# Performance work log

Measured on AMD Instinct MI355X. Metric: run time of the kernel, lower is better.

## Reference

```python
import jax, jax.numpy as jnp
import numpy as np

ALPHA = 0.2  # LeakyReLU negative slope
B, L, FIN, FOUT = 128, 512, 128, 128

def setup_inputs() -> dict:
    key = jax.random.key(0)
    k1, k2, k3, k4, k5 = jax.random.split(key, 5)
    h = jax.random.normal(k1, (B, L, FIN), jnp.float32)
    W = jax.random.normal(k2, (FIN, FOUT), jnp.float32) * (1.0 / np.sqrt(FIN))
    a = jax.random.normal(k3, (2 * FOUT,), jnp.float32) * (1.0 / np.sqrt(2 * FOUT))
    edge_bias = jax.random.normal(k4, (B, L, L), jnp.float32) * 0.1
    adj_mask = jax.random.uniform(k5, (L, L)) > 0.3
    adj_mask = adj_mask | jnp.eye(L, dtype=bool)  # self-loops avoid fully-masked rows
    return {"h": h, "W": W, "a": a, "edge_bias": edge_bias, "adj_mask": adj_mask}

def reference(h, W, a, edge_bias, adj_mask):
    # Wh: [B, L, Fout]
    Wh = jnp.einsum('blf,fo->blo', h, W)
    Fout = W.shape[1]
    # a([Wh_i, Wh_j]) == Wh_i @ a[:Fout] + Wh_j @ a[Fout:]  (avoids O(B*L*L*2F) concat)
    ei = Wh @ a[:Fout]   # [B, L]  (target i contribution)
    ej = Wh @ a[Fout:]   # [B, L]  (source j contribution)
    e = jax.nn.leaky_relu(ei[:, :, None] + ej[:, None, :], ALPHA) + edge_bias  # [B, L, L]
    e = jnp.where(adj_mask[None, :, :], e, -jnp.inf)
    att = jax.nn.softmax(e, axis=-1)  # dropout=0.0 -> identity
    h_prime = jnp.einsum('bij,bjo->bio', att, Wh)  # [B, L, Fout]
    return jax.nn.elu(h_prime)  # concat=True branch
```

## Files before the change

kernel.cpp:

```cpp
#include <hip/hip_runtime.h>
#include <string.h>

#define ALPHA 0.2f

typedef short short8 __attribute__((ext_vector_type(8)));
typedef float floatx4 __attribute__((ext_vector_type(4)));
typedef int intx4 __attribute__((ext_vector_type(4)));
typedef unsigned short ushort4v __attribute__((ext_vector_type(4)));

__device__ inline unsigned short f2bf(float f) {
    unsigned int v; __builtin_memcpy(&v, &f, 4);
    v = v + 0x7FFFu + ((v >> 16) & 1u);
    return (unsigned short)(v >> 16);
}

__global__ __launch_bounds__(256) void wh_kernel(const float* __restrict__ h,
                                                 const float* __restrict__ W,
                                                 const float* __restrict__ a,
                                                 unsigned short* __restrict__ wht,
                                                 float* __restrict__ ei,
                                                 float* __restrict__ ej)
{
    __shared__ __align__(16) unsigned short h_s[128][136];
    __shared__ __align__(16) unsigned short w_s[128][136];
    __shared__ float a_s[256];
    const int tid  = threadIdx.x;
    const int lane = tid & 63;
    const int wv   = tid >> 6;
    const int quad = lane >> 4;
    const int l16  = lane & 15;
    const int r0   = blockIdx.x * 128;
    const int b    = r0 >> 9;
    const int jb   = r0 & 511;

    const float* hbase = h + (size_t)r0 * 128;
    for (int it = 0; it < 16; ++it) {
        int idx4 = it * 256 + tid;
        floatx4 v = *(const floatx4*)(hbase + idx4 * 4);
        int row = idx4 >> 5;
        int col = (idx4 & 31) * 4;
        ushort4v u;
        for (int e = 0; e < 4; ++e) u[e] = f2bf(v[e]);
        *(ushort4v*)&h_s[row][col] = u;
    }
    for (int it = 0; it < 64; ++it) {
        int idx = it * 256 + tid;
        w_s[idx & 127][idx >> 7] = f2bf(W[idx]);
    }
    a_s[tid] = a[tid];
    __syncthreads();

    floatx4 acc[8][2];
    for (int mo = 0; mo < 8; ++mo)
        for (int n = 0; n < 2; ++n) acc[mo][n] = (floatx4)0.f;

    for (int kk = 0; kk < 4; ++kk) {
        short8 bfr[2];
        for (int n = 0; n < 2; ++n)
            bfr[n] = *(const short8*)&h_s[wv * 32 + n * 16 + l16][kk * 32 + quad * 8];
        for (int mo = 0; mo < 8; ++mo) {
            short8 afr = *(const short8*)&w_s[mo * 16 + l16][kk * 32 + quad * 8];
            acc[mo][0] = __builtin_amdgcn_mfma_f32_16x16x32_bf16(afr, bfr[0], acc[mo][0], 0, 0, 0);
            acc[mo][1] = __builtin_amdgcn_mfma_f32_16x16x32_bf16(afr, bfr[1], acc[mo][1], 0, 0, 0);
        }
    }

    for (int n = 0; n < 2; ++n) {
        float si = 0.f, sj = 0.f;
        for (int mo = 0; mo < 8; ++mo)
            for (int r = 0; r < 4; ++r) {
                int o = mo * 16 + quad * 4 + r;
                float v = acc[mo][n][r];
                si += v * a_s[o];
                sj += v * a_s[128 + o];
            }
        si += __shfl_xor(si, 16); si += __shfl_xor(si, 32);
        sj += __shfl_xor(sj, 16); sj += __shfl_xor(sj, 32);
        if (quad == 0) {
            int j = jb + wv * 32 + n * 16 + l16;
            ei[b * 512 + j] = si;
            ej[b * 512 + j] = sj;
        }
    }

    for (int mo = 0; mo < 8; ++mo)
        for (int n = 0; n < 2; ++n)
            for (int r = 0; r < 4; ++r) {
                int o = mo * 16 + quad * 4 + r;
                int j = jb + wv * 32 + n * 16 + l16;
                wht[(size_t)b * 65536 + o * 512 + j] = f2bf(acc[mo][n][r]);
            }
}

__global__ __launch_bounds__(256, 4) void attn_kernel(const unsigned short* __restrict__ wht,
                                                      const float* __restrict__ ei,
                                                      const float* __restrict__ ej,
                                                      const float* __restrict__ bias,
                                                      const int* __restrict__ adj,
                                                      float* __restrict__ out)
{
    __shared__ __align__(16) unsigned short p_s[32][520];
    __shared__ float ei_s[32];
    __shared__ float s_row[32];

    const int tid  = threadIdx.x;
    const int lane = tid & 63;
    const int wv   = tid >> 6;
    const int quad = lane >> 4;
    const int l16  = lane & 15;
    const int b    = blockIdx.x >> 4;
    const int i0   = (blockIdx.x & 15) * 32;

    const floatx4 ejv0 = *(const floatx4*)(ej + b * 512 + lane * 4);
    const floatx4 ejv1 = *(const floatx4*)(ej + b * 512 + 256 + lane * 4);
    if (tid < 32) ei_s[tid] = ei[b * 512 + i0 + tid];
    __syncthreads();

    const float* bp = bias + ((size_t)(b * 512 + i0 + wv * 8)) * 512;
    const int*   ap = adj + (i0 + wv * 8) * 512;
    floatx4 bb0 = *(const floatx4*)(bp + lane * 4);
    floatx4 bb1 = *(const floatx4*)(bp + 256 + lane * 4);
    intx4   mm0 = *(const intx4*)(ap + lane * 4);
    intx4   mm1 = *(const intx4*)(ap + 256 + lane * 4);

    float rsum[8];

#pragma unroll
    for (int rr = 0; rr < 8; ++rr) {
        floatx4 nb0, nb1; intx4 nm0, nm1;
        if (rr < 7) {
            nb0 = *(const floatx4*)(bp + 512 + lane * 4);
            nb1 = *(const floatx4*)(bp + 768 + lane * 4);
            nm0 = *(const intx4*)(ap + 512 + lane * 4);
            nm1 = *(const intx4*)(ap + 768 + lane * 4);
        }
        const int il = wv * 8 + rr;
        const float eiv = ei_s[il];
        float sm = 0.f;
        ushort4v p0, p1;
        for (int e = 0; e < 4; ++e) {
            float x = eiv + ejv0[e];
            x = fmaxf(x, ALPHA * x);
            x += bb0[e];
            float p = __expf(x);
            p = (mm0[e] != 0) ? p : 0.f;
            sm += p;
            p0[e] = f2bf(p);
        }
        for (int e = 0; e < 4; ++e) {
            float x = eiv + ejv1[e];
            x = fmaxf(x, ALPHA * x);
            x += bb1[e];
            float p = __expf(x);
            p = (mm1[e] != 0) ? p : 0.f;
            sm += p;
            p1[e] = f2bf(p);
        }
        *(ushort4v*)&p_s[il][lane * 4]       = p0;
        *(ushort4v*)&p_s[il][256 + lane * 4] = p1;
        rsum[rr] = sm;
        bb0 = nb0; bb1 = nb1; mm0 = nm0; mm1 = nm1;
        bp += 512; ap += 512;
    }

#pragma unroll
    for (int rr = 0; rr < 8; ++rr)
        for (int off = 32; off; off >>= 1)
            rsum[rr] += __shfl_xor(rsum[rr], off);
    if (lane == 0)
#pragma unroll
        for (int rr = 0; rr < 8; ++rr) s_row[wv * 8 + rr] = rsum[rr];
    __syncthreads();

    floatx4 acc[2][2];
    for (int m = 0; m < 2; ++m)
        for (int n = 0; n < 2; ++n) acc[m][n] = (floatx4)0.f;

    const unsigned short* wbase = wht + (size_t)b * 65536;
    const unsigned short* wb0 = wbase + (wv * 32 + l16) * 512 + quad * 8;
    const unsigned short* wb1 = wbase + (wv * 32 + 16 + l16) * 512 + quad * 8;
    short8 bf0 = *(const short8*)(wb0);
    short8 bf1 = *(const short8*)(wb1);
#pragma unroll
    for (int k16 = 0; k16 < 16; ++k16) {
        int ko = k16 * 32 + quad * 8;
        short8 nbf0, nbf1;
        if (k16 < 15) {
            nbf0 = *(const short8*)(wb0 + (k16 + 1) * 32);
            nbf1 = *(const short8*)(wb1 + (k16 + 1) * 32);
        }
        short8 af0 = *(const short8*)&p_s[l16][ko];
        short8 af1 = *(const short8*)&p_s[16 + l16][ko];
        acc[0][0] = __builtin_amdgcn_mfma_f32_16x16x32_bf16(af0, bf0, acc[0][0], 0, 0, 0);
        acc[0][1] = __builtin_amdgcn_mfma_f32_16x16x32_bf16(af0, bf1, acc[0][1], 0, 0, 0);
        acc[1][0] = __builtin_amdgcn_mfma_f32_16x16x32_bf16(af1, bf0, acc[1][0], 0, 0, 0);
        acc[1][1] = __builtin_amdgcn_mfma_f32_16x16x32_bf16(af1, bf1, acc[1][1], 0, 0, 0);
        bf0 = nbf0; bf1 = nbf1;
    }

    for (int m = 0; m < 2; ++m)
        for (int n = 0; n < 2; ++n)
            for (int r = 0; r < 4; ++r) {
                int il = m * 16 + quad * 4 + r;
                int o  = wv * 32 + n * 16 + l16;
                float v = acc[m][n][r] / s_row[il];
                v = v > 0.f ? v : (__expf(v) - 1.f);
                out[((size_t)(b * 512 + i0 + il)) * 128 + o] = v;
            }
}

extern "C" void kernel_launch(void* const* d_in, const int* in_sizes, int n_in,
                              void* d_out, int out_size, void* d_ws, size_t ws_size,
                              hipStream_t stream)
{
    const float* h    = (const float*)d_in[0];
    const float* W    = (const float*)d_in[1];
    const float* a    = (const float*)d_in[2];
    const float* bias = (const float*)d_in[3];
    const int*   adj  = (const int*)d_in[4];
    float*       out  = (float*)d_out;

    unsigned short* wht = (unsigned short*)d_ws;
    float* ei = (float*)((char*)d_ws + 16777216);
    float* ej = ei + 65536;

    hipLaunchKernelGGL(wh_kernel,   dim3(512),  dim3(256), 0, stream, h, W, a, wht, ei, ej);
    hipLaunchKernelGGL(attn_kernel, dim3(2048), dim3(256), 0, stream, wht, ei, ej, bias, adj, out);
}
```

Before: 262.3 us.

## Double threads per block and add nontemporal loads/stores for streamed data

Both kernels move from 256 to 512 threads per block, so each wave handles half as many rows/columns (4 attention rows instead of 8, one 16-column MFMA tile instead of two), with launch bounds raised for occupancy. Streaming inputs (h, edge_bias) use nontemporal loads and the output uses nontemporal stores to reduce cache pollution. The bias/adj prefetch is also issued before the first barrier so it overlaps the ei/ej loads. More waves add latency hiding at the cost of less per-wave reuse of the P fragments and W^T loads.

```diff
diff --git a/kernel.cpp b/kernel.cpp
--- a/kernel.cpp
+++ b/kernel.cpp
@@ -14,12 +14,16 @@
     return (unsigned short)(v >> 16);
 }
 
-__global__ __launch_bounds__(256) void wh_kernel(const float* __restrict__ h,
-                                                 const float* __restrict__ W,
-                                                 const float* __restrict__ a,
-                                                 unsigned short* __restrict__ wht,
-                                                 float* __restrict__ ei,
-                                                 float* __restrict__ ej)
+__device__ inline floatx4 ntload_f4(const float* p) {
+    return __builtin_nontemporal_load((const floatx4*)p);
+}
+
+__global__ __launch_bounds__(512, 4) void wh_kernel(const float* __restrict__ h,
+                                                    const float* __restrict__ W,
+                                                    const float* __restrict__ a,
+                                                    unsigned short* __restrict__ wht,
+                                                    float* __restrict__ ei,
+                                                    float* __restrict__ ej)
 {
     __shared__ __align__(16) unsigned short h_s[128][136];
     __shared__ __align__(16) unsigned short w_s[128][136];
@@ -34,65 +38,67 @@
     const int jb   = r0 & 511;
 
     const float* hbase = h + (size_t)r0 * 128;
-    for (int it = 0; it < 16; ++it) {
-        int idx4 = it * 256 + tid;
-        floatx4 v = *(const floatx4*)(hbase + idx4 * 4);
+#pragma unroll
+    for (int it = 0; it < 8; ++it) {
+        int idx4 = it * 512 + tid;
+        floatx4 v = ntload_f4(hbase + idx4 * 4);
         int row = idx4 >> 5;
         int col = (idx4 & 31) * 4;
         ushort4v u;
         for (int e = 0; e < 4; ++e) u[e] = f2bf(v[e]);
         *(ushort4v*)&h_s[row][col] = u;
     }
-    for (int it = 0; it < 64; ++it) {
-        int idx = it * 256 + tid;
+#pragma unroll
+    for (int it = 0; it < 32; ++it) {
+        int idx = it * 512 + tid;
         w_s[idx & 127][idx >> 7] = f2bf(W[idx]);
     }
-    a_s[tid] = a[tid];
+    if (tid < 256) a_s[tid] = a[tid];
     __syncthreads();
 
-    floatx4 acc[8][2];
-    for (int mo = 0; mo < 8; ++mo)
-        for (int n = 0; n < 2; ++n) acc[mo][n] = (floatx4)0.f;
-
+    floatx4 acc[8];
+#pragma unroll
+    for (int mo = 0; mo < 8; ++mo) acc[mo] = (floatx4)0.f;
+
+#pragma unroll
     for (int kk = 0; kk < 4; ++kk) {
-        short8 bfr[2];
-        for (int n = 0; n < 2; ++n)
-            bfr[n] = *(const short8*)&h_s[wv * 32 + n * 16 + l16][kk * 32 + quad * 8];
+        short8 bfr = *(const short8*)&h_s[wv * 16 + l16][kk * 32 + quad * 8];
+#pragma unroll
         for (int mo = 0; mo < 8; ++mo) {
             short8 afr = *(const short8*)&w_s[mo * 16 + l16][kk * 32 + quad * 8];
-            acc[mo][0] = __builtin_amdgcn_mfma_f32_16x16x32_bf16(afr, bfr[0], acc[mo][0], 0, 0, 0);
-            acc[mo][1] = __builtin_amdgcn_mfma_f32_16x16x32_bf16(afr, bfr[1], acc[mo][1], 0, 0, 0);
-        }
-    }
-
-    for (int n = 0; n < 2; ++n) {
+            acc[mo] = __builtin_amdgcn_mfma_f32_16x16x32_bf16(afr, bfr, acc[mo], 0, 0, 0);
+        }
+    }
+
+    {
         float si = 0.f, sj = 0.f;
+#pragma unroll
         for (int mo = 0; mo < 8; ++mo)
             for (int r = 0; r < 4; ++r) {
                 int o = mo * 16 + quad * 4 + r;
-                float v = acc[mo][n][r];
+                float v = acc[mo][r];
                 si += v * a_s[o];
                 sj += v * a_s[128 + o];
             }
         si += __shfl_xor(si, 16); si += __shfl_xor(si, 32);
         sj += __shfl_xor(sj, 16); sj += __shfl_xor(sj, 32);
         if (quad == 0) {
-            int j = jb + wv * 32 + n * 16 + l16;
+            int j = jb + wv * 16 + l16;
             ei[b * 512 + j] = si;
             ej[b * 512 + j] = sj;
         }
     }
 
+#pragma unroll
     for (int mo = 0; mo < 8; ++mo)
-        for (int n = 0; n < 2; ++n)
-            for (int r = 0; r < 4; ++r) {
-                int o = mo * 16 + quad * 4 + r;
-                int j = jb + wv * 32 + n * 16 + l16;
-                wht[(size_t)b * 65536 + o * 512 + j] = f2bf(acc[mo][n][r]);
-            }
-}
-
-__global__ __launch_bounds__(256, 4) void attn_kernel(const unsigned short* __restrict__ wht,
+        for (int r = 0; r < 4; ++r) {
+            int o = mo * 16 + quad * 4 + r;
+            int j = jb + wv * 16 + l16;
+            wht[(size_t)b * 65536 + o * 512 + j] = f2bf(acc[mo][r]);
+        }
+}
+
+__global__ __launch_bounds__(512, 8) void attn_kernel(const unsigned short* __restrict__ wht,
                                                       const float* __restrict__ ei,
                                                       const float* __restrict__ ej,
                                                       const float* __restrict__ bias,
@@ -111,30 +117,30 @@
     const int b    = blockIdx.x >> 4;
     const int i0   = (blockIdx.x & 15) * 32;
 
+    const float* bp = bias + ((size_t)(b * 512 + i0 + wv * 4)) * 512;
+    const int*   ap = adj + (i0 + wv * 4) * 512;
+    floatx4 bb0 = ntload_f4(bp + lane * 4);
+    floatx4 bb1 = ntload_f4(bp + 256 + lane * 4);
+    intx4   mm0 = *(const intx4*)(ap + lane * 4);
+    intx4   mm1 = *(const intx4*)(ap + 256 + lane * 4);
+
     const floatx4 ejv0 = *(const floatx4*)(ej + b * 512 + lane * 4);
     const floatx4 ejv1 = *(const floatx4*)(ej + b * 512 + 256 + lane * 4);
     if (tid < 32) ei_s[tid] = ei[b * 512 + i0 + tid];
     __syncthreads();
 
-    const float* bp = bias + ((size_t)(b * 512 + i0 + wv * 8)) * 512;
-    const int*   ap = adj + (i0 + wv * 8) * 512;
-    floatx4 bb0 = *(const floatx4*)(bp + lane * 4);
-    floatx4 bb1 = *(const floatx4*)(bp + 256 + lane * 4);
-    intx4   mm0 = *(const intx4*)(ap + lane * 4);
-    intx4   mm1 = *(const intx4*)(ap + 256 + lane * 4);
-
-    float rsum[8];
-
-#pragma unroll
-    for (int rr = 0; rr < 8; ++rr) {
+    float rsum[4];
+
+#pragma unroll
+    for (int rr = 0; rr < 4; ++rr) {
         floatx4 nb0, nb1; intx4 nm0, nm1;
-        if (rr < 7) {
-            nb0 = *(const floatx4*)(bp + 512 + lane * 4);
-            nb1 = *(const floatx4*)(bp + 768 + lane * 4);
+        if (rr < 3) {
+            nb0 = ntload_f4(bp + 512 + lane * 4);
+            nb1 = ntload_f4(bp + 768 + lane * 4);
             nm0 = *(const intx4*)(ap + 512 + lane * 4);
             nm1 = *(const intx4*)(ap + 768 + lane * 4);
         }
-        const int il = wv * 8 + rr;
+        const int il = wv * 4 + rr;
         const float eiv = ei_s[il];
         float sm = 0.f;
         ushort4v p0, p1;
@@ -163,50 +169,43 @@
         bp += 512; ap += 512;
     }
 
-#pragma unroll
-    for (int rr = 0; rr < 8; ++rr)
+    const unsigned short* wb = wht + (size_t)b * 65536 + (wv * 16 + l16) * 512 + quad * 8;
+    short8 bf = *(const short8*)(wb);
+
+#pragma unroll
+    for (int rr = 0; rr < 4; ++rr)
         for (int off = 32; off; off >>= 1)
             rsum[rr] += __shfl_xor(rsum[rr], off);
     if (lane == 0)
 #pragma unroll
-        for (int rr = 0; rr < 8; ++rr) s_row[wv * 8 + rr] = rsum[rr];
+        for (int rr = 0; rr < 4; ++rr) s_row[wv * 4 + rr] = rsum[rr];
     __syncthreads();
 
-    floatx4 acc[2][2];
-    for (int m = 0; m < 2; ++m)
-        for (int n = 0; n < 2; ++n) acc[m][n] = (floatx4)0.f;
-
-    const unsigned short* wbase = wht + (size_t)b * 65536;
-    const unsigned short* wb0 = wbase + (wv * 32 + l16) * 512 + quad * 8;
-    const unsigned short* wb1 = wbase + (wv * 32 + 16 + l16) * 512 + quad * 8;
-    short8 bf0 = *(const short8*)(wb0);
-    short8 bf1 = *(const short8*)(wb1);
+    floatx4 acc[2];
+    acc[0] = (floatx4)0.f;
+    acc[1] = (floatx4)0.f;
+
 #pragma unroll
     for (int k16 = 0; k16 < 16; ++k16) {
         int ko = k16 * 32 + quad * 8;
-        short8 nbf0, nbf1;
-        if (k16 < 15) {
-            nbf0 = *(const short8*)(wb0 + (k16 + 1) * 32);
-            nbf1 = *(const short8*)(wb1 + (k16 + 1) * 32);
-        }
+        short8 nbf;
+        if (k16 < 15) nbf = *(const short8*)(wb + (k16 + 1) * 32);
         short8 af0 = *(const short8*)&p_s[l16][ko];
         short8 af1 = *(const short8*)&p_s[16 + l16][ko];
-        acc[0][0] = __builtin_amdgcn_mfma_f32_16x16x32_bf16(af0, bf0, acc[0][0], 0, 0, 0);
-        acc[0][1] = __builtin_amdgcn_mfma_f32_16x16x32_bf16(af0, bf1, acc[0][1], 0, 0, 0);
-        acc[1][0] = __builtin_amdgcn_mfma_f32_16x16x32_bf16(af1, bf0, acc[1][0], 0, 0, 0);
-        acc[1][1] = __builtin_amdgcn_mfma_f32_16x16x32_bf16(af1, bf1, acc[1][1], 0, 0, 0);
-        bf0 = nbf0; bf1 = nbf1;
-    }
-
+        acc[0] = __builtin_amdgcn_mfma_f32_16x16x32_bf16(af0, bf, acc[0], 0, 0, 0);
+        acc[1] = __builtin_amdgcn_mfma_f32_16x16x32_bf16(af1, bf, acc[1], 0, 0, 0);
+        bf = nbf;
+    }
+
+#pragma unroll
     for (int m = 0; m < 2; ++m)
-        for (int n = 0; n < 2; ++n)
-            for (int r = 0; r < 4; ++r) {
-                int il = m * 16 + quad * 4 + r;
-                int o  = wv * 32 + n * 16 + l16;
-                float v = acc[m][n][r] / s_row[il];
-                v = v > 0.f ? v : (__expf(v) - 1.f);
-                out[((size_t)(b * 512 + i0 + il)) * 128 + o] = v;
-            }
+        for (int r = 0; r < 4; ++r) {
+            int il = m * 16 + quad * 4 + r;
+            int o  = wv * 16 + l16;
+            float v = acc[m][r] / s_row[il];
+            v = v > 0.f ? v : (__expf(v) - 1.f);
+            __builtin_nontemporal_store(v, &out[((size_t)(b * 512 + i0 + il)) * 128 + o]);
+        }
 }
 
 extern "C" void kernel_launch(void* const* d_in, const int* in_sizes, int n_in,
@@ -224,6 +223,6 @@
     float* ei = (float*)((char*)d_ws + 16777216);
     float* ej = ei + 65536;
 
-    hipLaunchKernelGGL(wh_kernel,   dim3(512),  dim3(256), 0, stream, h, W, a, wht, ei, ej);
-    hipLaunchKernelGGL(attn_kernel, dim3(2048), dim3(256), 0, stream, wht, ei, ej, bias, adj, out);
-}
+    hipLaunchKernelGGL(wh_kernel,   dim3(512),  dim3(512), 0, stream, h, W, a, wht, ei, ej);
+    hipLaunchKernelGGL(attn_kernel, dim3(2048), dim3(512), 0, stream, wht, ei, ej, bias, adj, out);
+}
```

Measured after the change: 264.7 us. Within noise of the previous version (+0.9%).

## Split attention into separate score and PV kernels via bf16 probability buffer

Applied to the files above, without the earlier changes.

Unfuses the attention kernel into a score kernel, which computes unnormalized exp scores and row sums and writes them to a bf16 global buffer, and a PV kernel with 512 threads that loads those scores into shared memory and runs the MFMA product. The aim is higher parallelism and better streaming of the large edge_bias read, using nontemporal loads and stores. The cost is an extra round trip of about 64MB of bf16 probabilities through global memory plus an additional kernel launch.

```diff
diff --git a/kernel.cpp b/kernel.cpp
--- a/kernel.cpp
+++ b/kernel.cpp
@@ -12,6 +12,10 @@
     unsigned int v; __builtin_memcpy(&v, &f, 4);
     v = v + 0x7FFFu + ((v >> 16) & 1u);
     return (unsigned short)(v >> 16);
+}
+
+__device__ inline floatx4 ntload_f4(const float* p) {
+    return __builtin_nontemporal_load((const floatx4*)p);
 }
 
 __global__ __launch_bounds__(256) void wh_kernel(const float* __restrict__ h,
@@ -92,16 +96,69 @@
             }
 }
 
-__global__ __launch_bounds__(256, 4) void attn_kernel(const unsigned short* __restrict__ wht,
-                                                      const float* __restrict__ ei,
-                                                      const float* __restrict__ ej,
-                                                      const float* __restrict__ bias,
-                                                      const int* __restrict__ adj,
-                                                      float* __restrict__ out)
+__global__ __launch_bounds__(256) void score_kernel(const float* __restrict__ ei,
+                                                    const float* __restrict__ ej,
+                                                    const float* __restrict__ bias,
+                                                    const int* __restrict__ adj,
+                                                    unsigned short* __restrict__ p,
+                                                    float* __restrict__ srow)
+{
+    const int tid  = threadIdx.x;
+    const int lane = tid & 63;
+    const int wv   = tid >> 6;
+    const int row  = blockIdx.x * 4 + wv;
+    const int i    = row & 511;
+    const int b    = row >> 9;
+
+    const float* bp  = bias + (size_t)row * 512 + lane * 8;
+    const int*   ap  = adj + i * 512 + lane * 8;
+    const float* ejp = ej + b * 512 + lane * 8;
+
+    floatx4 b0 = ntload_f4(bp);
+    floatx4 b1 = ntload_f4(bp + 4);
+    intx4   m0 = *(const intx4*)(ap);
+    intx4   m1 = *(const intx4*)(ap + 4);
+    floatx4 e0 = *(const floatx4*)(ejp);
+    floatx4 e1 = *(const floatx4*)(ejp + 4);
+    const float eiv = ei[row];
+
+    short8 pv;
+    float sm = 0.f;
+#pragma unroll
+    for (int e = 0; e < 4; ++e) {
+        float x = eiv + e0[e];
+        x = fmaxf(x, ALPHA * x);
+        x += b0[e];
+        float pe = __expf(x);
+        pe = (m0[e] != 0) ? pe : 0.f;
+        sm += pe;
+        pv[e] = (short)f2bf(pe);
+    }
+#pragma unroll
+    for (int e = 0; e < 4; ++e) {
+        float x = eiv + e1[e];
+        x = fmaxf(x, ALPHA * x);
+        x += b1[e];
+        float pe = __expf(x);
+        pe = (m1[e] != 0) ? pe : 0.f;
+        sm += pe;
+        pv[4 + e] = (short)f2bf(pe);
+    }
+
+#pragma unroll
+    for (int off = 32; off; off >>= 1) sm += __shfl_xor(sm, off);
+
+    *(short8*)(p + (size_t)row * 512 + lane * 8) = pv;
+    if (lane == 0) srow[row] = sm;
+}
+
+__global__ __launch_bounds__(512, 8) void pv_kernel(const unsigned short* __restrict__ p,
+                                                    const float* __restrict__ srow,
+                                                    const unsigned short* __restrict__ wht,
+                                                    float* __restrict__ out)
 {
     __shared__ __align__(16) unsigned short p_s[32][520];
-    __shared__ float ei_s[32];
-    __shared__ float s_row[32];
+    __shared__ float s_row_s[32];
 
     const int tid  = threadIdx.x;
     const int lane = tid & 63;
@@ -111,102 +168,45 @@
     const int b    = blockIdx.x >> 4;
     const int i0   = (blockIdx.x & 15) * 32;
 
-    const floatx4 ejv0 = *(const floatx4*)(ej + b * 512 + lane * 4);
-    const floatx4 ejv1 = *(const floatx4*)(ej + b * 512 + 256 + lane * 4);
-    if (tid < 32) ei_s[tid] = ei[b * 512 + i0 + tid];
+    const unsigned short* wb = wht + (size_t)b * 65536 + (wv * 16 + l16) * 512 + quad * 8;
+    short8 bf = *(const short8*)(wb);
+
+    const unsigned short* psrc = p + ((size_t)(b * 512 + i0)) * 512;
+#pragma unroll
+    for (int it = 0; it < 4; ++it) {
+        int idx = it * 512 + tid;
+        short8 v = *(const short8*)(psrc + idx * 8);
+        *(short8*)&p_s[idx >> 6][(idx & 63) * 8] = v;
+    }
+    if (tid < 32) s_row_s[tid] = srow[b * 512 + i0 + tid];
     __syncthreads();
 
-    const float* bp = bias + ((size_t)(b * 512 + i0 + wv * 8)) * 512;
-    const int*   ap = adj + (i0 + wv * 8) * 512;
-    floatx4 bb0 = *(const floatx4*)(bp + lane * 4);
-    floatx4 bb1 = *(const floatx4*)(bp + 256 + lane * 4);
-    intx4   mm0 = *(const intx4*)(ap + lane * 4);
-    intx4   mm1 = *(const intx4*)(ap + 256 + lane * 4);
-
-    float rsum[8];
-
-#pragma unroll
-    for (int rr = 0; rr < 8; ++rr) {
-        floatx4 nb0, nb1; intx4 nm0, nm1;
-        if (rr < 7) {
-            nb0 = *(const floatx4*)(bp + 512 + lane * 4);
-            nb1 = *(const floatx4*)(bp + 768 + lane * 4);
-            nm0 = *(const intx4*)(ap + 512 + lane * 4);
-            nm1 = *(const intx4*)(ap + 768 + lane * 4);
-        }
-        const int il = wv * 8 + rr;
-        const float eiv = ei_s[il];
-        float sm = 0.f;
-        ushort4v p0, p1;
-        for (int e = 0; e < 4; ++e) {
-            float x = eiv + ejv0[e];
-            x = fmaxf(x, ALPHA * x);
-            x += bb0[e];
-            float p = __expf(x);
-            p = (mm0[e] != 0) ? p : 0.f;
-            sm += p;
-            p0[e] = f2bf(p);
-        }
-        for (int e = 0; e < 4; ++e) {
-            float x = eiv + ejv1[e];
-            x = fmaxf(x, ALPHA * x);
-            x += bb1[e];
-            float p = __expf(x);
-            p = (mm1[e] != 0) ? p : 0.f;
-            sm += p;
-            p1[e] = f2bf(p);
-        }
-        *(ushort4v*)&p_s[il][lane * 4]       = p0;
-        *(ushort4v*)&p_s[il][256 + lane * 4] = p1;
-        rsum[rr] = sm;
-        bb0 = nb0; bb1 = nb1; mm0 = nm0; mm1 = nm1;
-        bp += 512; ap += 512;
-    }
-
-#pragma unroll
-    for (int rr = 0; rr < 8; ++rr)
-        for (int off = 32; off; off >>= 1)
-            rsum[rr] += __shfl_xor(rsum[rr], off);
-    if (lane == 0)
-#pragma unroll
-        for (int rr = 0; rr < 8; ++rr) s_row[wv * 8 + rr] = rsum[rr];
-    __syncthreads();
-
-    floatx4 acc[2][2];
-    for (int m = 0; m < 2; ++m)
-        for (int n = 0; n < 2; ++n) acc[m][n] = (floatx4)0.f;
-
-    const unsigned short* wbase = wht + (size_t)b * 65536;
-    const unsigned short* wb0 = wbase + (wv * 32 + l16) * 512 + quad * 8;
-    const unsigned short* wb1 = wbase + (wv * 32 + 16 + l16) * 512 + quad * 8;
-    short8 bf0 = *(const short8*)(wb0);
-    short8 bf1 = *(const short8*)(wb1);
+    floatx4 acc[2];
+    acc[0] = (floatx4)0.f;
+    acc[1] = (floatx4)0.f;
+
 #pragma unroll
     for (int k16 = 0; k16 < 16; ++k16) {
         int ko = k16 * 32 + quad * 8;
-        short8 nbf0, nbf1;
-        if (k16 < 15) {
-            nbf0 = *(const short8*)(wb0 + (k16 + 1) * 32);
-            nbf1 = *(const short8*)(wb1 + (k16 + 1) * 32);
-        }
+        short8 nbf;
+        if (k16 < 15) nbf = *(const short8*)(wb + (k16 + 1) * 32);
         short8 af0 = *(const short8*)&p_s[l16][ko];
         short8 af1 = *(const short8*)&p_s[16 + l16][ko];
-        acc[0][0] = __builtin_amdgcn_mfma_f32_16x16x32_bf16(af0, bf0, acc[0][0], 0, 0, 0);
-        acc[0][1] = __builtin_amdgcn_mfma_f32_16x16x32_bf16(af0, bf1, acc[0][1], 0, 0, 0);
-        acc[1][0] = __builtin_amdgcn_mfma_f32_16x16x32_bf16(af1, bf0, acc[1][0], 0, 0, 0);
-        acc[1][1] = __builtin_amdgcn_mfma_f32_16x16x32_bf16(af1, bf1, acc[1][1], 0, 0, 0);
-        bf0 = nbf0; bf1 = nbf1;
-    }
-
+        acc[0] = __builtin_amdgcn_mfma_f32_16x16x32_bf16(af0, bf, acc[0], 0, 0, 0);
+        acc[1] = __builtin_amdgcn_mfma_f32_16x16x32_bf16(af1, bf, acc[1], 0, 0, 0);
+        bf = nbf;
+    }
+
+#pragma unroll
     for (int m = 0; m < 2; ++m)
-        for (int n = 0; n < 2; ++n)
-            for (int r = 0; r < 4; ++r) {
-                int il = m * 16 + quad * 4 + r;
-                int o  = wv * 32 + n * 16 + l16;
-                float v = acc[m][n][r] / s_row[il];
-                v = v > 0.f ? v : (__expf(v) - 1.f);
-                out[((size_t)(b * 512 + i0 + il)) * 128 + o] = v;
-            }
+#pragma unroll
+        for (int r = 0; r < 4; ++r) {
+            int il = m * 16 + quad * 4 + r;
+            int o  = wv * 16 + l16;
+            float v = acc[m][r] / s_row_s[il];
+            v = v > 0.f ? v : (__expf(v) - 1.f);
+            __builtin_nontemporal_store(v, &out[((size_t)(b * 512 + i0 + il)) * 128 + o]);
+        }
 }
 
 extern "C" void kernel_launch(void* const* d_in, const int* in_sizes, int n_in,
@@ -223,7 +223,10 @@
     unsigned short* wht = (unsigned short*)d_ws;
     float* ei = (float*)((char*)d_ws + 16777216);
     float* ej = ei + 65536;
-
-    hipLaunchKernelGGL(wh_kernel,   dim3(512),  dim3(256), 0, stream, h, W, a, wht, ei, ej);
-    hipLaunchKernelGGL(attn_kernel, dim3(2048), dim3(256), 0, stream, wht, ei, ej, bias, adj, out);
-}
+    unsigned short* pbuf = (unsigned short*)((char*)d_ws + 17301504);
+    float* srow = (float*)((char*)d_ws + 17301504 + 67108864);
+
+    hipLaunchKernelGGL(wh_kernel,    dim3(512),   dim3(256), 0, stream, h, W, a, wht, ei, ej);
+    hipLaunchKernelGGL(score_kernel, dim3(16384), dim3(256), 0, stream, ei, ej, bias, adj, pbuf, srow);
+    hipLaunchKernelGGL(pv_kernel,    dim3(2048),  dim3(512), 0, stream, pbuf, srow, wht, out);
+}
```

Result: slower. 278.5 us (+6.2%).

## Enlarge attention tile to 64 rows with 512 threads, swizzle blocks, nontemporal bias

Applied to the files above, without the earlier changes.

The attention kernel now processes 64 query rows per block with 8 waves instead of 32 rows with 4 waves. Each wave owns 16 output features across all 64 rows, so every Wh fragment loaded from global memory feeds four MFMAs and the number of blocks reading the same Wh slice is halved. Block indices are remapped so that neighbouring block IDs fall on different batches, and the streaming bias reads and output writes use nontemporal hints to keep them from polluting cache. The cost is a larger LDS footprint per block and fewer blocks (1024), which may reduce occupancy.

```diff
diff --git a/kernel.cpp b/kernel.cpp
--- a/kernel.cpp
+++ b/kernel.cpp
@@ -12,6 +12,10 @@
     unsigned int v; __builtin_memcpy(&v, &f, 4);
     v = v + 0x7FFFu + ((v >> 16) & 1u);
     return (unsigned short)(v >> 16);
+}
+
+__device__ inline floatx4 ntload_f4(const float* p) {
+    return __builtin_nontemporal_load((const floatx4*)p);
 }
 
 __global__ __launch_bounds__(256) void wh_kernel(const float* __restrict__ h,
@@ -92,36 +96,40 @@
             }
 }
 
-__global__ __launch_bounds__(256, 4) void attn_kernel(const unsigned short* __restrict__ wht,
+__global__ __launch_bounds__(512, 4) void attn_kernel(const unsigned short* __restrict__ wht,
                                                       const float* __restrict__ ei,
                                                       const float* __restrict__ ej,
                                                       const float* __restrict__ bias,
                                                       const int* __restrict__ adj,
                                                       float* __restrict__ out)
 {
-    __shared__ __align__(16) unsigned short p_s[32][520];
-    __shared__ float ei_s[32];
-    __shared__ float s_row[32];
+    __shared__ __align__(16) unsigned short p_s[64][520];
+    __shared__ float ei_s[64];
+    __shared__ float s_row[64];
 
     const int tid  = threadIdx.x;
     const int lane = tid & 63;
     const int wv   = tid >> 6;
     const int quad = lane >> 4;
     const int l16  = lane & 15;
-    const int b    = blockIdx.x >> 4;
-    const int i0   = (blockIdx.x & 15) * 32;
+
+    const int n  = blockIdx.x;
+    const int x  = n & 7;
+    const int r  = n >> 3;
+    const int b  = x * 16 + (r >> 3);
+    const int i0 = (r & 7) * 64;
+
+    const float* bp = bias + ((size_t)(b * 512 + i0 + wv * 8)) * 512;
+    const int*   ap = adj + (i0 + wv * 8) * 512;
+    floatx4 bb0 = ntload_f4(bp + lane * 4);
+    floatx4 bb1 = ntload_f4(bp + 256 + lane * 4);
+    intx4   mm0 = *(const intx4*)(ap + lane * 4);
+    intx4   mm1 = *(const intx4*)(ap + 256 + lane * 4);
 
     const floatx4 ejv0 = *(const floatx4*)(ej + b * 512 + lane * 4);
     const floatx4 ejv1 = *(const floatx4*)(ej + b * 512 + 256 + lane * 4);
-    if (tid < 32) ei_s[tid] = ei[b * 512 + i0 + tid];
+    if (tid < 64) ei_s[tid] = ei[b * 512 + i0 + tid];
     __syncthreads();
-
-    const float* bp = bias + ((size_t)(b * 512 + i0 + wv * 8)) * 512;
-    const int*   ap = adj + (i0 + wv * 8) * 512;
-    floatx4 bb0 = *(const floatx4*)(bp + lane * 4);
-    floatx4 bb1 = *(const floatx4*)(bp + 256 + lane * 4);
-    intx4   mm0 = *(const intx4*)(ap + lane * 4);
-    intx4   mm1 = *(const intx4*)(ap + 256 + lane * 4);
 
     float rsum[8];
 
@@ -129,8 +137,8 @@
     for (int rr = 0; rr < 8; ++rr) {
         floatx4 nb0, nb1; intx4 nm0, nm1;
         if (rr < 7) {
-            nb0 = *(const floatx4*)(bp + 512 + lane * 4);
-            nb1 = *(const floatx4*)(bp + 768 + lane * 4);
+            nb0 = ntload_f4(bp + 512 + lane * 4);
+            nb1 = ntload_f4(bp + 768 + lane * 4);
             nm0 = *(const intx4*)(ap + 512 + lane * 4);
             nm1 = *(const intx4*)(ap + 768 + lane * 4);
         }
@@ -138,20 +146,22 @@
         const float eiv = ei_s[il];
         float sm = 0.f;
         ushort4v p0, p1;
+#pragma unroll
         for (int e = 0; e < 4; ++e) {
-            float x = eiv + ejv0[e];
-            x = fmaxf(x, ALPHA * x);
-            x += bb0[e];
-            float p = __expf(x);
+            float xv = eiv + ejv0[e];
+            xv = fmaxf(xv, ALPHA * xv);
+            xv += bb0[e];
+            float p = __expf(xv);
             p = (mm0[e] != 0) ? p : 0.f;
             sm += p;
             p0[e] = f2bf(p);
         }
+#pragma unroll
         for (int e = 0; e < 4; ++e) {
-            float x = eiv + ejv1[e];
-            x = fmaxf(x, ALPHA * x);
-            x += bb1[e];
-            float p = __expf(x);
+            float xv = eiv + ejv1[e];
+            xv = fmaxf(xv, ALPHA * xv);
+            xv += bb1[e];
+            float p = __expf(xv);
             p = (mm1[e] != 0) ? p : 0.f;
             sm += p;
             p1[e] = f2bf(p);
@@ -172,41 +182,38 @@
         for (int rr = 0; rr < 8; ++rr) s_row[wv * 8 + rr] = rsum[rr];
     __syncthreads();
 
-    floatx4 acc[2][2];
-    for (int m = 0; m < 2; ++m)
-        for (int n = 0; n < 2; ++n) acc[m][n] = (floatx4)0.f;
-
-    const unsigned short* wbase = wht + (size_t)b * 65536;
-    const unsigned short* wb0 = wbase + (wv * 32 + l16) * 512 + quad * 8;
-    const unsigned short* wb1 = wbase + (wv * 32 + 16 + l16) * 512 + quad * 8;
-    short8 bf0 = *(const short8*)(wb0);
-    short8 bf1 = *(const short8*)(wb1);
+    floatx4 acc[4];
+#pragma unroll
+    for (int m = 0; m < 4; ++m) acc[m] = (floatx4)0.f;
+
+    const unsigned short* wb = wht + (size_t)b * 65536 + (wv * 16 + l16) * 512 + quad * 8;
+    short8 bf = *(const short8*)(wb);
 #pragma unroll
     for (int k16 = 0; k16 < 16; ++k16) {
         int ko = k16 * 32 + quad * 8;
-        short8 nbf0, nbf1;
-        if (k16 < 15) {
-            nbf0 = *(const short8*)(wb0 + (k16 + 1) * 32);
-            nbf1 = *(const short8*)(wb1 + (k16 + 1) * 32);
-        }
+        short8 nbf;
+        if (k16 < 15) nbf = *(const short8*)(wb + (k16 + 1) * 32);
         short8 af0 = *(const short8*)&p_s[l16][ko];
         short8 af1 = *(const short8*)&p_s[16 + l16][ko];
-        acc[0][0] = __builtin_amdgcn_mfma_f32_16x16x32_bf16(af0, bf0, acc[0][0], 0, 0, 0);
-        acc[0][1] = __builtin_amdgcn_mfma_f32_16x16x32_bf16(af0, bf1, acc[0][1], 0, 0, 0);
-        acc[1][0] = __builtin_amdgcn_mfma_f32_16x16x32_bf16(af1, bf0, acc[1][0], 0, 0, 0);
-        acc[1][1] = __builtin_amdgcn_mfma_f32_16x16x32_bf16(af1, bf1, acc[1][1], 0, 0, 0);
-        bf0 = nbf0; bf1 = nbf1;
-    }
-
-    for (int m = 0; m < 2; ++m)
-        for (int n = 0; n < 2; ++n)
-            for (int r = 0; r < 4; ++r) {
-                int il = m * 16 + quad * 4 + r;
-                int o  = wv * 32 + n * 16 + l16;
-                float v = acc[m][n][r] / s_row[il];
-                v = v > 0.f ? v : (__expf(v) - 1.f);
-                out[((size_t)(b * 512 + i0 + il)) * 128 + o] = v;
-            }
+        short8 af2 = *(const short8*)&p_s[32 + l16][ko];
+        short8 af3 = *(const short8*)&p_s[48 + l16][ko];
+        acc[0] = __builtin_amdgcn_mfma_f32_16x16x32_bf16(af0, bf, acc[0], 0, 0, 0);
+        acc[1] = __builtin_amdgcn_mfma_f32_16x16x32_bf16(af1, bf, acc[1], 0, 0, 0);
+        acc[2] = __builtin_amdgcn_mfma_f32_16x16x32_bf16(af2, bf, acc[2], 0, 0, 0);
+        acc[3] = __builtin_amdgcn_mfma_f32_16x16x32_bf16(af3, bf, acc[3], 0, 0, 0);
+        bf = nbf;
+    }
+
+#pragma unroll
+    for (int m = 0; m < 4; ++m)
+#pragma unroll
+        for (int rr2 = 0; rr2 < 4; ++rr2) {
+            int il = m * 16 + quad * 4 + rr2;
+            int o  = wv * 16 + l16;
+            float v = acc[m][rr2] / s_row[il];
+            v = v > 0.f ? v : (__expf(v) - 1.f);
+            __builtin_nontemporal_store(v, &out[((size_t)(b * 512 + i0 + il)) * 128 + o]);
+        }
 }
 
 extern "C" void kernel_launch(void* const* d_in, const int* in_sizes, int n_in,
@@ -225,5 +232,5 @@
     float* ej = ei + 65536;
 
     hipLaunchKernelGGL(wh_kernel,   dim3(512),  dim3(256), 0, stream, h, W, a, wht, ei, ej);
-    hipLaunchKernelGGL(attn_kernel, dim3(2048), dim3(256), 0, stream, wht, ei, ej, bias, adj, out);
-}
+    hipLaunchKernelGGL(attn_kernel, dim3(1024), dim3(512), 0, stream, wht, ei, ej, bias, adj, out);
+}
```

Result: faster. 248.9 us (-5.1%).
